# Optimization experiments

Hardware: AMD Instinct MI355X
Metric: run time of the kernel (lower is better)

The kernel has to match this reference:

```python
import jax, jax.numpy as jnp
import numpy as np

N, K, D = 64, 512, 256
LEAKY_SLOPE = 0.01  # torch LeakyReLU default


def setup_inputs() -> dict:
    key = jax.random.key(0)
    k_x, k_w, k_b, k_aw, k_ab = jax.random.split(key, 5)
    x = jax.random.normal(k_x, (N, K, D), dtype=jnp.float32)
    # nn.Linear(D, D): weight [D, D], bias [D]
    W_w = jax.random.normal(k_w, (D, D), dtype=jnp.float32) / np.sqrt(D)
    W_b = jax.random.normal(k_b, (D,), dtype=jnp.float32) * 0.01
    # nn.Linear(2D, 1): weight [2D] (squeezed), bias scalar
    att_w = jax.random.normal(k_aw, (2 * D,), dtype=jnp.float32) / np.sqrt(2 * D)
    att_b = jax.random.normal(k_ab, (), dtype=jnp.float32) * 0.01
    return {"x": x, "W_w": W_w, "W_b": W_b, "att_w": att_w, "att_b": att_b}


def reference(x, W_w, W_b, att_w, att_b):
    n, k, d = x.shape
    # h = W(x): [N,K,D]
    h = jnp.einsum('nkd,ed->nke', x, W_w) + W_b
    # attention score e[n,i,j] = leaky_relu(concat(h_i, h_j) @ att_w + b)
    # split att_w to avoid materializing the [N,K,K,2D] concat tensor
    s_src = h @ att_w[:d]   # [N,K] contribution of h_i (first half of concat)
    s_dst = h @ att_w[d:]   # [N,K] contribution of h_j (second half)
    e = jax.nn.leaky_relu(s_src[:, :, None] + s_dst[:, None, :] + att_b,
                          negative_slope=LEAKY_SLOPE)  # [N,K,K]
    a = jax.nn.softmax(e, axis=2)
    # faithful to original einsum 'nkj,nkd->nkd' (sums attention over j,
    # then scales h elementwise)
    out = jnp.einsum('nkj,nkd->nkd', a, h)
    return jax.nn.relu(out)
```

## Files before the change

kernel.cpp:

```cpp
#include <hip/hip_runtime.h>
#include <hip/hip_bf16.h>


#define DD 256
#define M_TOTAL 32768
#define LW_STRIDE 264

typedef short bf16x8 __attribute__((ext_vector_type(8)));
typedef float floatx16 __attribute__((ext_vector_type(16)));

__device__ inline bf16x8 pack8(float4 p0, float4 p1) {
    __hip_bfloat162 q0 = __float22bfloat162_rn(make_float2(p0.x, p0.y));
    __hip_bfloat162 q1 = __float22bfloat162_rn(make_float2(p0.z, p0.w));
    __hip_bfloat162 q2 = __float22bfloat162_rn(make_float2(p1.x, p1.y));
    __hip_bfloat162 q3 = __float22bfloat162_rn(make_float2(p1.z, p1.w));
    union { bf16x8 v; unsigned u[4]; } r;
    union { __hip_bfloat162 h; unsigned u; } c;
    c.h = q0; r.u[0] = c.u;
    c.h = q1; r.u[1] = c.u;
    c.h = q2; r.u[2] = c.u;
    c.h = q3; r.u[3] = c.u;
    return r.v;
}

__global__ void __launch_bounds__(256, 4)
fcgat_gemm(const float* __restrict__ x, const float* __restrict__ W,
           const float* __restrict__ Wbias, float* __restrict__ out) {
    __shared__ __align__(16) unsigned short lw[64 * LW_STRIDE];

    const int tid  = threadIdx.x;
    const int lane = tid & 63;
    const int wave = tid >> 6;
    const int ln   = lane & 31;
    const int lh   = lane >> 5;
    const int mblk = blockIdx.x >> 2;
    const int e0   = (blockIdx.x & 3) * 64;
    const int m0   = mblk * 128 + wave * 32;

    const float* xb = x + (m0 + ln) * DD + lh * 8;

    float4 buf[8][2];
#pragma unroll
    for (int s = 0; s < 8; ++s) {
        buf[s][0] = *(const float4*)(xb + s * 16);
        buf[s][1] = *(const float4*)(xb + s * 16 + 4);
    }

    {
        const int r = tid >> 2;
        const int q = tid & 3;
        const float* src = W + (e0 + r) * DD + q * 64;
        unsigned short* dst = lw + r * LW_STRIDE + q * 64;
#pragma unroll
        for (int i = 0; i < 8; ++i) {
            float4 a0 = *(const float4*)(src + i * 8);
            float4 a1 = *(const float4*)(src + i * 8 + 4);
            *(bf16x8*)(dst + i * 8) = pack8(a0, a1);
        }
    }
    __syncthreads();

    floatx16 acc0, acc1;
#pragma unroll
    for (int i = 0; i < 16; ++i) { acc0[i] = 0.f; acc1[i] = 0.f; }

    const unsigned short* lb0 = lw + ln * LW_STRIDE + lh * 8;
    const unsigned short* lb1 = lb0 + 32 * LW_STRIDE;

#pragma unroll
    for (int s = 0; s < 16; ++s) {
        bf16x8 a  = pack8(buf[s & 7][0], buf[s & 7][1]);
        bf16x8 B0 = *(const bf16x8*)(lb0 + s * 16);
        bf16x8 B1 = *(const bf16x8*)(lb1 + s * 16);
        if (s + 8 < 16) {
            buf[s & 7][0] = *(const float4*)(xb + (s + 8) * 16);
            buf[s & 7][1] = *(const float4*)(xb + (s + 8) * 16 + 4);
        }
        acc0 = __builtin_amdgcn_mfma_f32_32x32x16_bf16(a, B0, acc0, 0, 0, 0);
        acc1 = __builtin_amdgcn_mfma_f32_32x32x16_bf16(a, B1, acc1, 0, 0, 0);
    }

    const float b0 = Wbias[e0 + ln];
    const float b1 = Wbias[e0 + 32 + ln];
    float* ob = out + e0 + ln;
#pragma unroll
    for (int r = 0; r < 16; ++r) {
        const int m = m0 + (r & 3) + 8 * (r >> 2) + 4 * lh;
        float v0 = acc0[r] + b0;
        float v1 = acc1[r] + b1;
        v0 = v0 > 0.f ? v0 : 0.f;
        v1 = v1 > 0.f ? v1 : 0.f;
        __builtin_nontemporal_store(v0, ob + m * DD);
        __builtin_nontemporal_store(v1, ob + m * DD + 32);
    }
}

extern "C" void kernel_launch(void* const* d_in, const int* in_sizes, int n_in,
                              void* d_out, int out_size, void* d_ws, size_t ws_size,
                              hipStream_t stream) {
    const float* x    = (const float*)d_in[0];
    const float* W_w  = (const float*)d_in[1];
    const float* W_b  = (const float*)d_in[2];
    float* out = (float*)d_out;

    fcgat_gemm<<<M_TOTAL / 128 * 4, 256, 0, stream>>>(x, W_w, W_b, out);
}
```

Before: 108.0 us.

## Stage x tile through LDS and split 64x64 tile across four waves

Reworks the GEMM tiling: each block now covers 64 rows by 64 output columns, loads both the x tile and W tile into LDS as bf16, and assigns each wave a 32x32 MFMA subtile. This replaces direct per-wave register prefetch of x with a shared staging step and doubles the grid size. It aims for more parallelism and simpler register use, but loses load/compute overlap, re-reads W more often, and lowers the occupancy hint.

```diff
diff --git a/kernel.cpp b/kernel.cpp
--- a/kernel.cpp
+++ b/kernel.cpp
@@ -4,7 +4,7 @@
 
 #define DD 256
 #define M_TOTAL 32768
-#define LW_STRIDE 264
+#define LWS 264
 
 typedef short bf16x8 __attribute__((ext_vector_type(8)));
 typedef float floatx16 __attribute__((ext_vector_type(16)));
@@ -23,75 +23,65 @@
     return r.v;
 }
 
-__global__ void __launch_bounds__(256, 4)
+__global__ void __launch_bounds__(256, 2)
 fcgat_gemm(const float* __restrict__ x, const float* __restrict__ W,
            const float* __restrict__ Wbias, float* __restrict__ out) {
-    __shared__ __align__(16) unsigned short lw[64 * LW_STRIDE];
+    __shared__ __align__(16) unsigned short lx[64 * LWS];
+    __shared__ __align__(16) unsigned short lw[64 * LWS];
 
-    const int tid  = threadIdx.x;
-    const int lane = tid & 63;
-    const int wave = tid >> 6;
-    const int ln   = lane & 31;
-    const int lh   = lane >> 5;
-    const int mblk = blockIdx.x >> 2;
-    const int e0   = (blockIdx.x & 3) * 64;
-    const int m0   = mblk * 128 + wave * 32;
-
-    const float* xb = x + (m0 + ln) * DD + lh * 8;
-
-    float4 buf[8][2];
-#pragma unroll
-    for (int s = 0; s < 8; ++s) {
-        buf[s][0] = *(const float4*)(xb + s * 16);
-        buf[s][1] = *(const float4*)(xb + s * 16 + 4);
-    }
+    const int tid = threadIdx.x;
+    const int bm  = blockIdx.x >> 2;
+    const int e0  = (blockIdx.x & 3) * 64;
+    const int m0  = bm * 64;
 
     {
-        const int r = tid >> 2;
-        const int q = tid & 3;
-        const float* src = W + (e0 + r) * DD + q * 64;
-        unsigned short* dst = lw + r * LW_STRIDE + q * 64;
+        const int sr = tid >> 5;
+        const int sc = (tid & 31) * 8;
+        const float* xs = x + (m0 + sr) * DD + sc;
+        const float* ws = W + (e0 + sr) * DD + sc;
+        unsigned short* dx = lx + sr * LWS + sc;
+        unsigned short* dw = lw + sr * LWS + sc;
 #pragma unroll
         for (int i = 0; i < 8; ++i) {
-            float4 a0 = *(const float4*)(src + i * 8);
-            float4 a1 = *(const float4*)(src + i * 8 + 4);
-            *(bf16x8*)(dst + i * 8) = pack8(a0, a1);
+            float4 a0 = *(const float4*)(xs + i * 8 * DD);
+            float4 a1 = *(const float4*)(xs + i * 8 * DD + 4);
+            float4 b0 = *(const float4*)(ws + i * 8 * DD);
+            float4 b1 = *(const float4*)(ws + i * 8 * DD + 4);
+            *(bf16x8*)(dx + i * 8 * LWS) = pack8(a0, a1);
+            *(bf16x8*)(dw + i * 8 * LWS) = pack8(b0, b1);
         }
     }
     __syncthreads();
 
-    floatx16 acc0, acc1;
+    const int lane = tid & 63;
+    const int wave = tid >> 6;
+    const int mw   = wave >> 1;
+    const int ew   = wave & 1;
+    const int ln   = lane & 31;
+    const int lh   = lane >> 5;
+
+    const unsigned short* ax = lx + (mw * 32 + ln) * LWS + lh * 8;
+    const unsigned short* bw = lw + (ew * 32 + ln) * LWS + lh * 8;
+
+    floatx16 acc;
 #pragma unroll
-    for (int i = 0; i < 16; ++i) { acc0[i] = 0.f; acc1[i] = 0.f; }
-
-    const unsigned short* lb0 = lw + ln * LW_STRIDE + lh * 8;
-    const unsigned short* lb1 = lb0 + 32 * LW_STRIDE;
+    for (int i = 0; i < 16; ++i) acc[i] = 0.f;
 
 #pragma unroll
     for (int s = 0; s < 16; ++s) {
-        bf16x8 a  = pack8(buf[s & 7][0], buf[s & 7][1]);
-        bf16x8 B0 = *(const bf16x8*)(lb0 + s * 16);
-        bf16x8 B1 = *(const bf16x8*)(lb1 + s * 16);
-        if (s + 8 < 16) {
-            buf[s & 7][0] = *(const float4*)(xb + (s + 8) * 16);
-            buf[s & 7][1] = *(const float4*)(xb + (s + 8) * 16 + 4);
-        }
-        acc0 = __builtin_amdgcn_mfma_f32_32x32x16_bf16(a, B0, acc0, 0, 0, 0);
-        acc1 = __builtin_amdgcn_mfma_f32_32x32x16_bf16(a, B1, acc1, 0, 0, 0);
+        bf16x8 af = *(const bf16x8*)(ax + s * 16);
+        bf16x8 bf = *(const bf16x8*)(bw + s * 16);
+        acc = __builtin_amdgcn_mfma_f32_32x32x16_bf16(af, bf, acc, 0, 0, 0);
     }
 
-    const float b0 = Wbias[e0 + ln];
-    const float b1 = Wbias[e0 + 32 + ln];
-    float* ob = out + e0 + ln;
+    const float bias = Wbias[e0 + ew * 32 + ln];
+    float* ob = out + e0 + ew * 32 + ln;
 #pragma unroll
     for (int r = 0; r < 16; ++r) {
-        const int m = m0 + (r & 3) + 8 * (r >> 2) + 4 * lh;
-        float v0 = acc0[r] + b0;
-        float v1 = acc1[r] + b1;
-        v0 = v0 > 0.f ? v0 : 0.f;
-        v1 = v1 > 0.f ? v1 : 0.f;
-        __builtin_nontemporal_store(v0, ob + m * DD);
-        __builtin_nontemporal_store(v1, ob + m * DD + 32);
+        const int m = m0 + mw * 32 + (r & 3) + 8 * (r >> 2) + 4 * lh;
+        float v = acc[r] + bias;
+        v = v > 0.f ? v : 0.f;
+        __builtin_nontemporal_store(v, ob + m * DD);
     }
 }
 
@@ -103,5 +93,5 @@
     const float* W_b  = (const float*)d_in[2];
     float* out = (float*)d_out;
 
-    fcgat_gemm<<<M_TOTAL / 128 * 4, 256, 0, stream>>>(x, W_w, W_b, out);
+    fcgat_gemm<<<(M_TOTAL / 64) * 4, 256, 0, stream>>>(x, W_w, W_b, out);
 }
```

After: 102.1 us. 5.5% less time.
